# Optimization experiments

Hardware: AMD Instinct MI355X
Metric: run time of the kernel (lower is better)

The kernel has to match this reference:

```python
import jax, jax.numpy as jnp
import numpy as np


def _sparsify24(w):
    """2:4 structured sparsity: per contiguous group of 4 along the last dim,
    keep the 2 largest-magnitude entries, zero the other 2 (soft_threshold24)."""
    m, n = w.shape
    g = w.reshape(m, n // 4, 4)
    a = jnp.abs(g)
    # 2nd-largest magnitude in each group = index 2 of ascending sort of 4
    thresh = jnp.sort(a, axis=-1)[..., 2:3]
    mask = a >= thresh
    return (g * mask).reshape(m, n)


def setup_inputs() -> dict:
    key = jax.random.key(0)
    k1, k2, k3 = jax.random.split(key, 3)
    B, S, DIN, DOUT = 4, 4096, 1024, 1024
    x = jax.random.normal(k1, (B, S, DIN), dtype=jnp.float32)
    weight = jax.random.normal(k2, (DIN, DOUT), dtype=jnp.float32) * 0.02
    bias = jax.random.normal(k3, (DOUT,), dtype=jnp.float32) * 0.02
    sparse_scale = jnp.ones((1,), dtype=jnp.float32)
    return {"x": x, "weight": weight, "bias": bias, "sparse_scale": sparse_scale}


def reference(x, weight, bias, sparse_scale):
    # get_sparse_weight: cast weight to fp16, apply 2:4 sparsity, multiply by
    # learnable fp32 scale (promotes to fp32 as in torch half*float).
    w_sparse = _sparsify24(weight.astype(jnp.float16)).astype(jnp.float32) * sparse_scale
    # fake_fp8_mm: both operands cast to fp16, accumulate/output in fp32.
    a = x.reshape(-1, x.shape[-1]).astype(jnp.float16)          # [B*S, DIN]
    b = w_sparse.astype(jnp.float16)                             # [DIN, DOUT]
    out = jnp.matmul(a, b, preferred_element_type=jnp.float32)   # [B*S, DOUT] fp32
    out = out.reshape(*x.shape[:-1], -1) + bias
    return out
```

## Files before the change

### kernel.cpp

```cpp
#include <hip/hip_runtime.h>
#include <hip/hip_fp16.h>
#include <stdint.h>

#define M_TOT 16384
#define N_TOT 1024
#define K_TOT 1024

typedef _Float16 f16x8 __attribute__((ext_vector_type(8)));
typedef float f32x4 __attribute__((ext_vector_type(4)));
typedef unsigned short ushort4v __attribute__((ext_vector_type(4)));

__device__ inline void gl2lds16(const void* g, void* l) {
    __builtin_amdgcn_global_load_lds(
        (const __attribute__((address_space(1))) void*)(uintptr_t)(g),
        (__attribute__((address_space(3))) void*)(uint32_t)(uintptr_t)(l),
        16, 0, 0);
}

__global__ void __launch_bounds__(256) prep_and_cast(const float* __restrict__ X,
                                                     const float* __restrict__ W,
                                                     const float* __restrict__ scale_p,
                                                     _Float16* __restrict__ Xh,
                                                     _Float16* __restrict__ wT) {
    const int tid = threadIdx.x;
    if (blockIdx.x < 256) {
        __shared__ _Float16 sT[64 * 68 + 4];
        const float scale = scale_p[0];
        const int k0 = (blockIdx.x & 15) * 64;
        const int n0 = (blockIdx.x >> 4) * 64;
        const int r = tid >> 4;
        const int c4 = (tid & 15) * 4;
#pragma unroll
        for (int p = 0; p < 4; ++p) {
            const int k = p * 16 + r;
            float4 w4 = *(const float4*)&W[(size_t)(k0 + k) * N_TOT + n0 + c4];
            _Float16 h0 = (_Float16)w4.x, h1 = (_Float16)w4.y, h2 = (_Float16)w4.z, h3 = (_Float16)w4.w;
            float a0 = fabsf((float)h0), a1 = fabsf((float)h1), a2 = fabsf((float)h2), a3 = fabsf((float)h3);
            float lo01 = fminf(a0, a1), hi01 = fmaxf(a0, a1);
            float lo23 = fminf(a2, a3), hi23 = fmaxf(a2, a3);
            float s2 = fmaxf(fminf(hi01, hi23), fmaxf(lo01, lo23));
            sT[(c4 + 0) * 68 + k] = (_Float16)(((a0 >= s2) ? (float)h0 : 0.0f) * scale);
            sT[(c4 + 1) * 68 + k] = (_Float16)(((a1 >= s2) ? (float)h1 : 0.0f) * scale);
            sT[(c4 + 2) * 68 + k] = (_Float16)(((a2 >= s2) ? (float)h2 : 0.0f) * scale);
            sT[(c4 + 3) * 68 + k] = (_Float16)(((a3 >= s2) ? (float)h3 : 0.0f) * scale);
        }
        __syncthreads();
#pragma unroll
        for (int p = 0; p < 4; ++p) {
            const int n = p * 16 + r;
            ushort4v v = *(const ushort4v*)&sT[n * 68 + c4];
            *(ushort4v*)&wT[(size_t)(n0 + n) * K_TOT + k0 + c4] = v;
        }
    } else {
        size_t i = ((size_t)(blockIdx.x - 256) * 256 + tid) * 8;
        float4 x0 = *(const float4*)&X[i];
        float4 x1 = *(const float4*)&X[i + 4];
        f16x8 h;
        h[0] = (_Float16)x0.x; h[1] = (_Float16)x0.y; h[2] = (_Float16)x0.z; h[3] = (_Float16)x0.w;
        h[4] = (_Float16)x1.x; h[5] = (_Float16)x1.y; h[6] = (_Float16)x1.z; h[7] = (_Float16)x1.w;
        *(f16x8*)&Xh[i] = h;
    }
}

__global__ void __launch_bounds__(512, 2) gemm_bt(const _Float16* __restrict__ A,
                                                  const _Float16* __restrict__ Bt,
                                                  const float* __restrict__ bias,
                                                  float* __restrict__ C) {
    __shared__ __align__(16) _Float16 sA[3][256 * 32];
    __shared__ __align__(16) _Float16 sB[3][256 * 32];

    const int tid = threadIdx.x;
    const int id = blockIdx.x;
    const int by = id & 63;
    const int bx = id >> 6;
    const int wave = tid >> 6;
    const int lane = tid & 63;
    const int wm = wave >> 2;
    const int wn = wave & 3;
    const int quad = lane >> 4;
    const int l16 = lane & 15;

    const int row0 = tid >> 2;
    const int s4 = tid & 3;
    const int g = s4 ^ ((row0 >> 1) & 3);
    const _Float16* gA = A + (size_t)(by * 256 + row0) * K_TOT + g * 8;
    const _Float16* gB = Bt + (size_t)(bx * 256 + row0) * K_TOT + g * 8;
    const int dst0 = row0 * 32 + s4 * 8;

    const int rdoff = l16 * 64 + ((quad ^ ((l16 >> 1) & 3)) << 4);

    f32x4 acc[8][4];
#pragma unroll
    for (int i = 0; i < 8; ++i)
#pragma unroll
        for (int j = 0; j < 4; ++j)
            acc[i][j] = (f32x4){0.f, 0.f, 0.f, 0.f};
    f16x8 fa[8], fb[4];

#define STAGE(t, b) do {                                                   \
        const _Float16* sa_ = gA + (size_t)(t) * 32;                       \
        gl2lds16(sa_, &sA[b][dst0]);                                       \
        gl2lds16(sa_ + (size_t)128 * K_TOT, &sA[b][dst0 + 128 * 32]);      \
        const _Float16* sb_ = gB + (size_t)(t) * 32;                       \
        gl2lds16(sb_, &sB[b][dst0]);                                       \
        gl2lds16(sb_ + (size_t)128 * K_TOT, &sB[b][dst0 + 128 * 32]);      \
    } while (0)
#define FENCE asm volatile("" ::: "memory")

#define PH(b, t2, b2, DO_STAGE, WLAST) do {                                        \
        if (WLAST) asm volatile("s_waitcnt vmcnt(0)" ::: "memory");                \
        else       asm volatile("s_waitcnt vmcnt(4)" ::: "memory");                \
        __builtin_amdgcn_sched_barrier(0);                                         \
        __builtin_amdgcn_s_barrier();                                              \
        FENCE;                                                                     \
        if (DO_STAGE) STAGE(t2, b2);                                               \
        {                                                                          \
            const char* bA_ = (const char*)&sA[b][0] + rdoff + wm * 8192;          \
            const char* bB_ = (const char*)&sB[b][0] + rdoff + wn * 4096;          \
            _Pragma("unroll")                                                      \
            for (int j = 0; j < 4; ++j) fb[j] = *(const f16x8*)(bB_ + j * 1024);   \
            _Pragma("unroll")                                                      \
            for (int i = 0; i < 8; ++i) fa[i] = *(const f16x8*)(bA_ + i * 1024);   \
        }                                                                          \
        __builtin_amdgcn_s_setprio(1);                                             \
        _Pragma("unroll")                                                          \
        for (int i = 0; i < 8; ++i) {                                              \
            _Pragma("unroll")                                                      \
            for (int j = 0; j < 4; ++j)                                            \
                acc[i][j] = __builtin_amdgcn_mfma_f32_16x16x32_f16(                \
                    fa[i], fb[j], acc[i][j], 0, 0, 0);                             \
        }                                                                          \
        __builtin_amdgcn_s_setprio(0);                                             \
    } while (0)

    STAGE(0, 0);
    STAGE(1, 1);

    for (int it = 0; it < 10; ++it) {
        const int t = 3 * it;
        PH(0, t + 2, 2, 1, 0);
        PH(1, t + 3, 0, 1, 0);
        PH(2, t + 4, 1, 1, 0);
    }
    PH(0, 0, 0, 0, 0);
    PH(1, 0, 0, 0, 1);

#pragma unroll
    for (int j = 0; j < 4; ++j) {
        const int col = bx * 256 + wn * 64 + j * 16 + l16;
        const float bj = bias[col];
#pragma unroll
        for (int mi = 0; mi < 8; ++mi) {
            const int row0o = by * 256 + wm * 128 + mi * 16 + quad * 4;
#pragma unroll
            for (int r = 0; r < 4; ++r) {
                C[(size_t)(row0o + r) * N_TOT + col] = acc[mi][j][r] + bj;
            }
        }
    }

#undef PH
#undef FENCE
#undef STAGE
}

extern "C" void kernel_launch(void* const* d_in, const int* in_sizes, int n_in,
                              void* d_out, int out_size, void* d_ws, size_t ws_size,
                              hipStream_t stream) {
    const float* x      = (const float*)d_in[0];
    const float* weight = (const float*)d_in[1];
    const float* bias   = (const float*)d_in[2];
    const float* sscale = (const float*)d_in[3];
    float* out = (float*)d_out;

    _Float16* wT = (_Float16*)d_ws;
    _Float16* xh = (_Float16*)((char*)d_ws + (size_t)2 * 1024 * 1024);

    prep_and_cast<<<256 + (M_TOT * K_TOT / 8) / 256, 256, 0, stream>>>(x, weight, sscale, xh, wT);
    gemm_bt<<<256, 512, 0, stream>>>(xh, wT, bias, out);
}
```

Measured before the change: 152.0 us.

## Fuse fp32-to-fp16 activation cast into GEMM A-tile loading

```diff
diff --git a/kernel.cpp b/kernel.cpp
--- a/kernel.cpp
+++ b/kernel.cpp
@@ -17,52 +17,40 @@
         16, 0, 0);
 }
 
-__global__ void __launch_bounds__(256) prep_and_cast(const float* __restrict__ X,
-                                                     const float* __restrict__ W,
-                                                     const float* __restrict__ scale_p,
-                                                     _Float16* __restrict__ Xh,
-                                                     _Float16* __restrict__ wT) {
+__global__ void __launch_bounds__(256) prep_w(const float* __restrict__ W,
+                                              const float* __restrict__ scale_p,
+                                              _Float16* __restrict__ wT) {
     const int tid = threadIdx.x;
-    if (blockIdx.x < 256) {
-        __shared__ _Float16 sT[64 * 68 + 4];
-        const float scale = scale_p[0];
-        const int k0 = (blockIdx.x & 15) * 64;
-        const int n0 = (blockIdx.x >> 4) * 64;
-        const int r = tid >> 4;
-        const int c4 = (tid & 15) * 4;
+    __shared__ _Float16 sT[64 * 68 + 4];
+    const float scale = scale_p[0];
+    const int k0 = (blockIdx.x & 15) * 64;
+    const int n0 = (blockIdx.x >> 4) * 64;
+    const int r = tid >> 4;
+    const int c4 = (tid & 15) * 4;
 #pragma unroll
-        for (int p = 0; p < 4; ++p) {
-            const int k = p * 16 + r;
-            float4 w4 = *(const float4*)&W[(size_t)(k0 + k) * N_TOT + n0 + c4];
-            _Float16 h0 = (_Float16)w4.x, h1 = (_Float16)w4.y, h2 = (_Float16)w4.z, h3 = (_Float16)w4.w;
-            float a0 = fabsf((float)h0), a1 = fabsf((float)h1), a2 = fabsf((float)h2), a3 = fabsf((float)h3);
-            float lo01 = fminf(a0, a1), hi01 = fmaxf(a0, a1);
-            float lo23 = fminf(a2, a3), hi23 = fmaxf(a2, a3);
-            float s2 = fmaxf(fminf(hi01, hi23), fmaxf(lo01, lo23));
-            sT[(c4 + 0) * 68 + k] = (_Float16)(((a0 >= s2) ? (float)h0 : 0.0f) * scale);
-            sT[(c4 + 1) * 68 + k] = (_Float16)(((a1 >= s2) ? (float)h1 : 0.0f) * scale);
-            sT[(c4 + 2) * 68 + k] = (_Float16)(((a2 >= s2) ? (float)h2 : 0.0f) * scale);
-            sT[(c4 + 3) * 68 + k] = (_Float16)(((a3 >= s2) ? (float)h3 : 0.0f) * scale);
-        }
-        __syncthreads();
+    for (int p = 0; p < 4; ++p) {
+        const int k = p * 16 + r;
+        float4 w4 = *(const float4*)&W[(size_t)(k0 + k) * N_TOT + n0 + c4];
+        _Float16 h0 = (_Float16)w4.x, h1 = (_Float16)w4.y, h2 = (_Float16)w4.z, h3 = (_Float16)w4.w;
+        float a0 = fabsf((float)h0), a1 = fabsf((float)h1), a2 = fabsf((float)h2), a3 = fabsf((float)h3);
+        float lo01 = fminf(a0, a1), hi01 = fmaxf(a0, a1);
+        float lo23 = fminf(a2, a3), hi23 = fmaxf(a2, a3);
+        float s2 = fmaxf(fminf(hi01, hi23), fmaxf(lo01, lo23));
+        sT[(c4 + 0) * 68 + k] = (_Float16)(((a0 >= s2) ? (float)h0 : 0.0f) * scale);
+        sT[(c4 + 1) * 68 + k] = (_Float16)(((a1 >= s2) ? (float)h1 : 0.0f) * scale);
+        sT[(c4 + 2) * 68 + k] = (_Float16)(((a2 >= s2) ? (float)h2 : 0.0f) * scale);
+        sT[(c4 + 3) * 68 + k] = (_Float16)(((a3 >= s2) ? (float)h3 : 0.0f) * scale);
+    }
+    __syncthreads();
 #pragma unroll
-        for (int p = 0; p < 4; ++p) {
-            const int n = p * 16 + r;
-            ushort4v v = *(const ushort4v*)&sT[n * 68 + c4];
-            *(ushort4v*)&wT[(size_t)(n0 + n) * K_TOT + k0 + c4] = v;
-        }
-    } else {
-        size_t i = ((size_t)(blockIdx.x - 256) * 256 + tid) * 8;
-        float4 x0 = *(const float4*)&X[i];
-        float4 x1 = *(const float4*)&X[i + 4];
-        f16x8 h;
-        h[0] = (_Float16)x0.x; h[1] = (_Float16)x0.y; h[2] = (_Float16)x0.z; h[3] = (_Float16)x0.w;
-        h[4] = (_Float16)x1.x; h[5] = (_Float16)x1.y; h[6] = (_Float16)x1.z; h[7] = (_Float16)x1.w;
-        *(f16x8*)&Xh[i] = h;
+    for (int p = 0; p < 4; ++p) {
+        const int n = p * 16 + r;
+        ushort4v v = *(const ushort4v*)&sT[n * 68 + c4];
+        *(ushort4v*)&wT[(size_t)(n0 + n) * K_TOT + k0 + c4] = v;
     }
 }
 
-__global__ void __launch_bounds__(512, 2) gemm_bt(const _Float16* __restrict__ A,
+__global__ void __launch_bounds__(512, 2) gemm_bt(const float* __restrict__ X,
                                                   const _Float16* __restrict__ Bt,
                                                   const float* __restrict__ bias,
                                                   float* __restrict__ C) {
@@ -83,9 +71,16 @@
     const int row0 = tid >> 2;
     const int s4 = tid & 3;
     const int g = s4 ^ ((row0 >> 1) & 3);
-    const _Float16* gA = A + (size_t)(by * 256 + row0) * K_TOT + g * 8;
     const _Float16* gB = Bt + (size_t)(bx * 256 + row0) * K_TOT + g * 8;
     const int dst0 = row0 * 32 + s4 * 8;
+
+    const int ar = tid >> 1;
+    const int ah = tid & 1;
+    const float* gX = X + (size_t)(by * 256 + ar) * K_TOT + ah * 16;
+    const int am = (ar >> 1) & 3;
+    const int aw0 = ar * 64 + (((2 * ah)     ^ am) << 4);
+    const int aw1 = ar * 64 + (((2 * ah + 1) ^ am) << 4);
+    float4 a0, a1, a2, a3;
 
     const int rdoff = l16 * 64 + ((quad ^ ((l16 >> 1) & 3)) << 4);
 
@@ -97,23 +92,36 @@
             acc[i][j] = (f32x4){0.f, 0.f, 0.f, 0.f};
     f16x8 fa[8], fb[4];
 
-#define STAGE(t, b) do {                                                   \
-        const _Float16* sa_ = gA + (size_t)(t) * 32;                       \
-        gl2lds16(sa_, &sA[b][dst0]);                                       \
-        gl2lds16(sa_ + (size_t)128 * K_TOT, &sA[b][dst0 + 128 * 32]);      \
+#define A_LOAD(t) do {                                                     \
+        const float* p_ = gX + (t) * 32;                                   \
+        a0 = *(const float4*)(p_);                                         \
+        a1 = *(const float4*)(p_ + 4);                                     \
+        a2 = *(const float4*)(p_ + 8);                                     \
+        a3 = *(const float4*)(p_ + 12);                                    \
+    } while (0)
+#define A_WRITE(wb) do {                                                   \
+        f16x8 lo_, hi_;                                                    \
+        lo_[0] = (_Float16)a0.x; lo_[1] = (_Float16)a0.y;                  \
+        lo_[2] = (_Float16)a0.z; lo_[3] = (_Float16)a0.w;                  \
+        lo_[4] = (_Float16)a1.x; lo_[5] = (_Float16)a1.y;                  \
+        lo_[6] = (_Float16)a1.z; lo_[7] = (_Float16)a1.w;                  \
+        hi_[0] = (_Float16)a2.x; hi_[1] = (_Float16)a2.y;                  \
+        hi_[2] = (_Float16)a2.z; hi_[3] = (_Float16)a2.w;                  \
+        hi_[4] = (_Float16)a3.x; hi_[5] = (_Float16)a3.y;                  \
+        hi_[6] = (_Float16)a3.z; hi_[7] = (_Float16)a3.w;                  \
+        *(f16x8*)((char*)&sA[wb][0] + aw0) = lo_;                          \
+        *(f16x8*)((char*)&sA[wb][0] + aw1) = hi_;                          \
+    } while (0)
+#define STAGE_B(t, b) do {                                                 \
         const _Float16* sb_ = gB + (size_t)(t) * 32;                       \
         gl2lds16(sb_, &sB[b][dst0]);                                       \
         gl2lds16(sb_ + (size_t)128 * K_TOT, &sB[b][dst0 + 128 * 32]);      \
     } while (0)
 #define FENCE asm volatile("" ::: "memory")
 
-#define PH(b, t2, b2, DO_STAGE, WLAST) do {                                        \
-        if (WLAST) asm volatile("s_waitcnt vmcnt(0)" ::: "memory");                \
-        else       asm volatile("s_waitcnt vmcnt(4)" ::: "memory");                \
-        __builtin_amdgcn_sched_barrier(0);                                         \
-        __builtin_amdgcn_s_barrier();                                              \
-        FENCE;                                                                     \
-        if (DO_STAGE) STAGE(t2, b2);                                               \
+#define PH(b, DO_W, wb, DO_S, t2, b2) do {                                         \
+        if (DO_W) A_WRITE(wb);                                                     \
+        if (DO_S) { STAGE_B(t2, b2); A_LOAD(t2); }                                 \
         {                                                                          \
             const char* bA_ = (const char*)&sA[b][0] + rdoff + wm * 8192;          \
             const char* bB_ = (const char*)&sB[b][0] + rdoff + wn * 4096;          \
@@ -131,19 +139,27 @@
                     fa[i], fb[j], acc[i][j], 0, 0, 0);                             \
         }                                                                          \
         __builtin_amdgcn_s_setprio(0);                                             \
+        asm volatile("s_waitcnt lgkmcnt(0)" ::: "memory");                         \
+        __builtin_amdgcn_s_barrier();                                              \
+        FENCE;                                                                     \
     } while (0)
 
-    STAGE(0, 0);
-    STAGE(1, 1);
+    A_LOAD(0);
+    STAGE_B(0, 0); STAGE_B(1, 1);
+    A_WRITE(0);
+    A_LOAD(1);
+    asm volatile("s_waitcnt lgkmcnt(0)" ::: "memory");
+    __builtin_amdgcn_s_barrier();
+    FENCE;
 
     for (int it = 0; it < 10; ++it) {
         const int t = 3 * it;
-        PH(0, t + 2, 2, 1, 0);
-        PH(1, t + 3, 0, 1, 0);
-        PH(2, t + 4, 1, 1, 0);
+        PH(0, 1, 1, 1, t + 2, 2);
+        PH(1, 1, 2, 1, t + 3, 0);
+        PH(2, 1, 0, 1, t + 4, 1);
     }
-    PH(0, 0, 0, 0, 0);
-    PH(1, 0, 0, 0, 1);
+    PH(0, 1, 1, 0, 0, 0);
+    PH(1, 0, 0, 0, 0, 0);
 
 #pragma unroll
     for (int j = 0; j < 4; ++j) {
@@ -161,7 +177,9 @@
 
 #undef PH
 #undef FENCE
-#undef STAGE
+#undef STAGE_B
+#undef A_WRITE
+#undef A_LOAD
 }
 
 extern "C" void kernel_launch(void* const* d_in, const int* in_sizes, int n_in,
@@ -174,8 +192,7 @@
     float* out = (float*)d_out;
 
     _Float16* wT = (_Float16*)d_ws;
-    _Float16* xh = (_Float16*)((char*)d_ws + (size_t)2 * 1024 * 1024);
 
-    prep_and_cast<<<256 + (M_TOT * K_TOT / 8) / 256, 256, 0, stream>>>(x, weight, sscale, xh, wT);
-    gemm_bt<<<256, 512, 0, stream>>>(xh, wT, bias, out);
+    prep_w<<<256, 256, 0, stream>>>(weight, sscale, wT);
+    gemm_bt<<<256, 512, 0, stream>>>(x, wT, bias, out);
 }
```

Result: slower. 168.4 us (+10.7%).

## Fuse fp32-to-fp16 activation cast into GEMM LDS load path

Applied to the files above, without the earlier changes.

```diff
diff --git a/kernel.cpp b/kernel.cpp
--- a/kernel.cpp
+++ b/kernel.cpp
@@ -17,57 +17,45 @@
         16, 0, 0);
 }
 
-__global__ void __launch_bounds__(256) prep_and_cast(const float* __restrict__ X,
-                                                     const float* __restrict__ W,
-                                                     const float* __restrict__ scale_p,
-                                                     _Float16* __restrict__ Xh,
-                                                     _Float16* __restrict__ wT) {
+__global__ void __launch_bounds__(256) prep_w(const float* __restrict__ W,
+                                              const float* __restrict__ scale_p,
+                                              _Float16* __restrict__ wT) {
     const int tid = threadIdx.x;
-    if (blockIdx.x < 256) {
-        __shared__ _Float16 sT[64 * 68 + 4];
-        const float scale = scale_p[0];
-        const int k0 = (blockIdx.x & 15) * 64;
-        const int n0 = (blockIdx.x >> 4) * 64;
-        const int r = tid >> 4;
-        const int c4 = (tid & 15) * 4;
+    __shared__ _Float16 sT[64 * 68 + 4];
+    const float scale = scale_p[0];
+    const int k0 = (blockIdx.x & 15) * 64;
+    const int n0 = (blockIdx.x >> 4) * 64;
+    const int r = tid >> 4;
+    const int c4 = (tid & 15) * 4;
 #pragma unroll
-        for (int p = 0; p < 4; ++p) {
-            const int k = p * 16 + r;
-            float4 w4 = *(const float4*)&W[(size_t)(k0 + k) * N_TOT + n0 + c4];
-            _Float16 h0 = (_Float16)w4.x, h1 = (_Float16)w4.y, h2 = (_Float16)w4.z, h3 = (_Float16)w4.w;
-            float a0 = fabsf((float)h0), a1 = fabsf((float)h1), a2 = fabsf((float)h2), a3 = fabsf((float)h3);
-            float lo01 = fminf(a0, a1), hi01 = fmaxf(a0, a1);
-            float lo23 = fminf(a2, a3), hi23 = fmaxf(a2, a3);
-            float s2 = fmaxf(fminf(hi01, hi23), fmaxf(lo01, lo23));
-            sT[(c4 + 0) * 68 + k] = (_Float16)(((a0 >= s2) ? (float)h0 : 0.0f) * scale);
-            sT[(c4 + 1) * 68 + k] = (_Float16)(((a1 >= s2) ? (float)h1 : 0.0f) * scale);
-            sT[(c4 + 2) * 68 + k] = (_Float16)(((a2 >= s2) ? (float)h2 : 0.0f) * scale);
-            sT[(c4 + 3) * 68 + k] = (_Float16)(((a3 >= s2) ? (float)h3 : 0.0f) * scale);
-        }
-        __syncthreads();
+    for (int p = 0; p < 4; ++p) {
+        const int k = p * 16 + r;
+        float4 w4 = *(const float4*)&W[(size_t)(k0 + k) * N_TOT + n0 + c4];
+        _Float16 h0 = (_Float16)w4.x, h1 = (_Float16)w4.y, h2 = (_Float16)w4.z, h3 = (_Float16)w4.w;
+        float a0 = fabsf((float)h0), a1 = fabsf((float)h1), a2 = fabsf((float)h2), a3 = fabsf((float)h3);
+        float lo01 = fminf(a0, a1), hi01 = fmaxf(a0, a1);
+        float lo23 = fminf(a2, a3), hi23 = fmaxf(a2, a3);
+        float s2 = fmaxf(fminf(hi01, hi23), fmaxf(lo01, lo23));
+        sT[(c4 + 0) * 68 + k] = (_Float16)(((a0 >= s2) ? (float)h0 : 0.0f) * scale);
+        sT[(c4 + 1) * 68 + k] = (_Float16)(((a1 >= s2) ? (float)h1 : 0.0f) * scale);
+        sT[(c4 + 2) * 68 + k] = (_Float16)(((a2 >= s2) ? (float)h2 : 0.0f) * scale);
+        sT[(c4 + 3) * 68 + k] = (_Float16)(((a3 >= s2) ? (float)h3 : 0.0f) * scale);
+    }
+    __syncthreads();
 #pragma unroll
-        for (int p = 0; p < 4; ++p) {
-            const int n = p * 16 + r;
-            ushort4v v = *(const ushort4v*)&sT[n * 68 + c4];
-            *(ushort4v*)&wT[(size_t)(n0 + n) * K_TOT + k0 + c4] = v;
-        }
-    } else {
-        size_t i = ((size_t)(blockIdx.x - 256) * 256 + tid) * 8;
-        float4 x0 = *(const float4*)&X[i];
-        float4 x1 = *(const float4*)&X[i + 4];
-        f16x8 h;
-        h[0] = (_Float16)x0.x; h[1] = (_Float16)x0.y; h[2] = (_Float16)x0.z; h[3] = (_Float16)x0.w;
-        h[4] = (_Float16)x1.x; h[5] = (_Float16)x1.y; h[6] = (_Float16)x1.z; h[7] = (_Float16)x1.w;
-        *(f16x8*)&Xh[i] = h;
+    for (int p = 0; p < 4; ++p) {
+        const int n = p * 16 + r;
+        ushort4v v = *(const ushort4v*)&sT[n * 68 + c4];
+        *(ushort4v*)&wT[(size_t)(n0 + n) * K_TOT + k0 + c4] = v;
     }
 }
 
-__global__ void __launch_bounds__(512, 2) gemm_bt(const _Float16* __restrict__ A,
+__global__ void __launch_bounds__(512, 2) gemm_bt(const float* __restrict__ X,
                                                   const _Float16* __restrict__ Bt,
                                                   const float* __restrict__ bias,
                                                   float* __restrict__ C) {
-    __shared__ __align__(16) _Float16 sA[3][256 * 32];
-    __shared__ __align__(16) _Float16 sB[3][256 * 32];
+    __shared__ __align__(16) float     sA[3][256 * 32];
+    __shared__ __align__(16) _Float16  sB[3][256 * 32];
 
     const int tid = threadIdx.x;
     const int id = blockIdx.x;
@@ -80,14 +68,22 @@
     const int quad = lane >> 4;
     const int l16 = lane & 15;
 
+    const int r0a = tid >> 3;
+    const int s8 = tid & 7;
+    const int g8 = s8 ^ (r0a & 7);
+    const float* gXs = X + (size_t)(by * 256 + r0a) * K_TOT + g8 * 4;
+    const int dstA = r0a * 32 + s8 * 4;
+
     const int row0 = tid >> 2;
     const int s4 = tid & 3;
     const int g = s4 ^ ((row0 >> 1) & 3);
-    const _Float16* gA = A + (size_t)(by * 256 + row0) * K_TOT + g * 8;
     const _Float16* gB = Bt + (size_t)(bx * 256 + row0) * K_TOT + g * 8;
-    const int dst0 = row0 * 32 + s4 * 8;
+    const int dstB = row0 * 32 + s4 * 8;
 
-    const int rdoff = l16 * 64 + ((quad ^ ((l16 >> 1) & 3)) << 4);
+    const int rdoffB = l16 * 64 + ((quad ^ ((l16 >> 1) & 3)) << 4);
+    const int e = l16 & 7;
+    const int rdA0 = l16 * 128 + (((2 * quad)     ^ e) << 4);
+    const int rdA1 = l16 * 128 + (((2 * quad + 1) ^ e) << 4);
 
     f32x4 acc[8][4];
 #pragma unroll
@@ -97,30 +93,41 @@
             acc[i][j] = (f32x4){0.f, 0.f, 0.f, 0.f};
     f16x8 fa[8], fb[4];
 
-#define STAGE(t, b) do {                                                   \
-        const _Float16* sa_ = gA + (size_t)(t) * 32;                       \
-        gl2lds16(sa_, &sA[b][dst0]);                                       \
-        gl2lds16(sa_ + (size_t)128 * K_TOT, &sA[b][dst0 + 128 * 32]);      \
-        const _Float16* sb_ = gB + (size_t)(t) * 32;                       \
-        gl2lds16(sb_, &sB[b][dst0]);                                       \
-        gl2lds16(sb_ + (size_t)128 * K_TOT, &sB[b][dst0 + 128 * 32]);      \
+#define STAGE(t, b) do {                                                    \
+        const float* sa_ = gXs + (size_t)(t) * 32;                          \
+        gl2lds16(sa_,                        &sA[b][dstA]);                 \
+        gl2lds16(sa_ + (size_t)64 * K_TOT,   &sA[b][dstA + 64 * 32]);       \
+        gl2lds16(sa_ + (size_t)128 * K_TOT,  &sA[b][dstA + 128 * 32]);      \
+        gl2lds16(sa_ + (size_t)192 * K_TOT,  &sA[b][dstA + 192 * 32]);      \
+        const _Float16* sb_ = gB + (size_t)(t) * 32;                        \
+        gl2lds16(sb_, &sB[b][dstB]);                                        \
+        gl2lds16(sb_ + (size_t)128 * K_TOT, &sB[b][dstB + 128 * 32]);       \
     } while (0)
 #define FENCE asm volatile("" ::: "memory")
 
 #define PH(b, t2, b2, DO_STAGE, WLAST) do {                                        \
         if (WLAST) asm volatile("s_waitcnt vmcnt(0)" ::: "memory");                \
-        else       asm volatile("s_waitcnt vmcnt(4)" ::: "memory");                \
+        else       asm volatile("s_waitcnt vmcnt(6)" ::: "memory");                \
         __builtin_amdgcn_sched_barrier(0);                                         \
         __builtin_amdgcn_s_barrier();                                              \
         FENCE;                                                                     \
         if (DO_STAGE) STAGE(t2, b2);                                               \
         {                                                                          \
-            const char* bA_ = (const char*)&sA[b][0] + rdoff + wm * 8192;          \
-            const char* bB_ = (const char*)&sB[b][0] + rdoff + wn * 4096;          \
+            const char* bB_ = (const char*)&sB[b][0] + rdoffB + wn * 4096;         \
             _Pragma("unroll")                                                      \
             for (int j = 0; j < 4; ++j) fb[j] = *(const f16x8*)(bB_ + j * 1024);   \
+            const char* bA_ = (const char*)&sA[b][0] + wm * 16384;                 \
             _Pragma("unroll")                                                      \
-            for (int i = 0; i < 8; ++i) fa[i] = *(const f16x8*)(bA_ + i * 1024);   \
+            for (int i = 0; i < 8; ++i) {                                          \
+                f32x4 u0 = *(const f32x4*)(bA_ + i * 2048 + rdA0);                 \
+                f32x4 u1 = *(const f32x4*)(bA_ + i * 2048 + rdA1);                 \
+                f16x8 t_;                                                          \
+                t_[0] = (_Float16)u0[0]; t_[1] = (_Float16)u0[1];                  \
+                t_[2] = (_Float16)u0[2]; t_[3] = (_Float16)u0[3];                  \
+                t_[4] = (_Float16)u1[0]; t_[5] = (_Float16)u1[1];                  \
+                t_[6] = (_Float16)u1[2]; t_[7] = (_Float16)u1[3];                  \
+                fa[i] = t_;                                                        \
+            }                                                                      \
         }                                                                          \
         __builtin_amdgcn_s_setprio(1);                                             \
         _Pragma("unroll")                                                          \
@@ -174,8 +181,7 @@
     float* out = (float*)d_out;
 
     _Float16* wT = (_Float16*)d_ws;
-    _Float16* xh = (_Float16*)((char*)d_ws + (size_t)2 * 1024 * 1024);
 
-    prep_and_cast<<<256 + (M_TOT * K_TOT / 8) / 256, 256, 0, stream>>>(x, weight, sscale, xh, wT);
-    gemm_bt<<<256, 512, 0, stream>>>(xh, wT, bias, out);
+    prep_w<<<256, 256, 0, stream>>>(weight, sscale, wT);
+    gemm_bt<<<256, 512, 0, stream>>>(x, wT, bias, out);
 }
```

Result: slower. 163.8 us (+7.7%).
